# Optimization experiments

Measured on AMD Instinct MI355X. Metric: run time of the kernel, lower is better.

The kernel has to match this reference:

```python
import jax, jax.numpy as jnp
import numpy as np
from math import pi

BS, H, C = 4096, 1024, 512
H2, C2 = H // 2, C // 2


def _cm(x, y):
    # complex multiply with real/imag stored in last dim
    return jnp.stack([x[..., 0] * y[..., 0] - x[..., 1] * y[..., 1],
                      x[..., 0] * y[..., 1] + x[..., 1] * y[..., 0]], -1)


def _interleave(a, b):
    # (H2, C2),(H2, C2) -> (H, C2) rows [a0,b0,a1,b1,...]
    return jnp.stack([a, b], 1).reshape(-1, a.shape[1])


def _rotations(phi, theta):
    cp, sp = jnp.cos(phi), jnp.sin(phi)
    ct, st = jnp.cos(theta), jnp.sin(theta)
    z = jnp.zeros_like(ct)
    diag = jnp.stack([_interleave(cp * ct, ct), _interleave(sp * ct, z)], -1)      # (H, C2, 2)
    offd = jnp.stack([_interleave(-cp * st, st), _interleave(-sp * st, z)], -1)    # (H, C2, 2)
    return diag.transpose(1, 0, 2), offd.transpose(1, 0, 2)                        # (C2, H, 2)


def _swap_pairs(x):
    # swap elements within adjacent pairs along the hidden axis
    bs, h, _ = x.shape
    return x.reshape(bs, h // 2, 2, 2)[:, :, ::-1, :].reshape(bs, h, 2)


def setup_inputs() -> dict:
    key = jax.random.key(0)
    ks = jax.random.split(key, 5)
    x = jax.random.normal(ks[0], (BS, H, 2), dtype=jnp.float32)
    phi0 = 2 * pi * jax.random.normal(ks[1], (H2, C2), dtype=jnp.float32)
    theta0 = 2 * pi * jax.random.normal(ks[2], (H2, C2), dtype=jnp.float32)
    phi1 = 2 * pi * jax.random.normal(ks[3], (H2, C2), dtype=jnp.float32)
    theta1 = 2 * pi * jax.random.normal(ks[4], (H2, C2), dtype=jnp.float32)
    return {"x": x, "phi0": phi0, "theta0": theta0, "phi1": phi1, "theta1": theta1}


def reference(x, phi0, theta0, phi1, theta1):
    d0, o0 = _rotations(phi0, theta0)
    d1, o1 = _rotations(phi1, theta1)

    def step(xc, dd):
        dd0, oo0, dd1, oo1 = dd
        xc = _cm(xc, dd0) + _cm(_swap_pairs(xc), oo0)
        xc = jnp.roll(xc, -1, axis=1)   # cat(x[1:], x[:1])
        xc = _cm(xc, dd1) + _cm(_swap_pairs(xc), oo1)
        xc = jnp.roll(xc, 1, axis=1)    # cat(x[-1:], x[:-1])
        return xc, None

    x, _ = jax.lax.scan(step, x, (d0, o0, d1, o1))
    return x
```

## Files before the change

### kernel.cpp

```cpp
#include <hip/hip_runtime.h>


#define H_DIM 1024
#define C2 256
#define RPW 2


__global__ __launch_bounds__(256) void eunn_coef_kernel(
    const float* __restrict__ phi0, const float* __restrict__ theta0,
    const float* __restrict__ phi1, const float* __restrict__ theta1,
    float4* __restrict__ coef) {
    int t = blockIdx.x * 256 + threadIdx.x;
    int i = t & 511;
    int p = (t >> 9) & 1;
    int c = t >> 10;
    const float* phi   = p ? phi1   : phi0;
    const float* theta = p ? theta1 : theta0;
    float ph = phi[i * C2 + c];
    float th = theta[i * C2 + c];
    float sp, cp, st, ct;
    __sincosf(ph, &sp, &cp);
    __sincosf(th, &st, &ct);
    int j = i & 7;
    int l = i >> 3;
    coef[(((c * 2 + p) * 8) + j) * 64 + l] = make_float4(ct, st, cp, sp);
}

__device__ __forceinline__ void rot_pair(const float4 q,
                                         float& ur, float& ui,
                                         float& wr, float& wi) {
    float ar = fmaf(-q.y, wr, q.x * ur);
    float ai = fmaf(-q.y, wi, q.x * ui);
    float br = fmaf( q.x, wr, q.y * ur);
    float bi = fmaf( q.x, wi, q.y * ui);
    ur = fmaf(-q.w, ai, q.z * ar);
    ui = fmaf( q.w, ar, q.z * ai);
    wr = br;
    wi = bi;
}

__global__ __launch_bounds__(256, 2) void eunn_main_kernel(
    const float* __restrict__ x,
    const float4* __restrict__ coef,
    float* __restrict__ out) {
    const int lane = threadIdx.x & 63;
    const int wave = threadIdx.x >> 6;
    const int row0 = (blockIdx.x * 4 + wave) * RPW;

    float vr[RPW][16], vi[RPW][16];

#pragma unroll
    for (int r = 0; r < RPW; ++r) {
        const float4* src = (const float4*)(x + (size_t)(row0 + r) * (H_DIM * 2)) + lane * 8;
#pragma unroll
        for (int m = 0; m < 8; ++m) {
            float4 f = src[m];
            vr[r][2 * m]     = f.x; vi[r][2 * m]     = f.y;
            vr[r][2 * m + 1] = f.z; vi[r][2 * m + 1] = f.w;
        }
    }

    const float4* cl = coef + lane;

#pragma unroll 1
    for (int c = 0; c < C2; ++c) {
        const float4* ca = cl + (size_t)c * 1024;

        float4 qq = ca[15 * 64];
        float qpx = __shfl(qq.x, (lane + 63) & 63);
        float qpy = __shfl(qq.y, (lane + 63) & 63);

        {
            float4 q0 = ca[0 * 64];
            float4 q7 = ca[7 * 64];
#pragma unroll
            for (int r = 0; r < RPW; ++r) {
                rot_pair(q0, vr[r][0],  vi[r][0],  vr[r][1],  vi[r][1]);
                rot_pair(q7, vr[r][14], vi[r][14], vr[r][15], vi[r][15]);
            }
        }
        float nbr[RPW], nbi[RPW], pbr[RPW], pbi[RPW];
#pragma unroll
        for (int r = 0; r < RPW; ++r) {
            nbr[r] = __shfl(vr[r][0],  (lane + 1)  & 63);
            nbi[r] = __shfl(vi[r][0],  (lane + 1)  & 63);
            pbr[r] = __shfl(vr[r][15], (lane + 63) & 63);
            pbi[r] = __shfl(vi[r][15], (lane + 63) & 63);
        }

#pragma unroll
        for (int j = 1; j < 7; ++j) {
            float4 q = ca[j * 64];
#pragma unroll
            for (int r = 0; r < RPW; ++r) {
                rot_pair(q, vr[r][2 * j],     vi[r][2 * j],
                            vr[r][2 * j + 1], vi[r][2 * j + 1]);
            }
        }

#pragma unroll
        for (int j = 0; j < 7; ++j) {
            float4 q = ca[(8 + j) * 64];
#pragma unroll
            for (int r = 0; r < RPW; ++r) {
                rot_pair(q, vr[r][2 * j + 1], vi[r][2 * j + 1],
                            vr[r][2 * j + 2], vi[r][2 * j + 2]);
            }
        }

#pragma unroll
        for (int r = 0; r < RPW; ++r) {
            float ar = fmaf(-qq.y, nbr[r], qq.x * vr[r][15]);
            float ai = fmaf(-qq.y, nbi[r], qq.x * vi[r][15]);
            vr[r][15] = fmaf(-qq.w, ai, qq.z * ar);
            vi[r][15] = fmaf( qq.w, ar, qq.z * ai);
            float b0r = fmaf(qpx, vr[r][0], qpy * pbr[r]);
            float b0i = fmaf(qpx, vi[r][0], qpy * pbi[r]);
            vr[r][0] = b0r; vi[r][0] = b0i;
        }
    }

#pragma unroll
    for (int r = 0; r < RPW; ++r) {
        float4* dst = (float4*)(out + (size_t)(row0 + r) * (H_DIM * 2)) + lane * 8;
#pragma unroll
        for (int m = 0; m < 8; ++m) {
            dst[m] = make_float4(vr[r][2 * m],     vi[r][2 * m],
                                 vr[r][2 * m + 1], vi[r][2 * m + 1]);
        }
    }
}

extern "C" void kernel_launch(void* const* d_in, const int* in_sizes, int n_in,
                              void* d_out, int out_size, void* d_ws, size_t ws_size,
                              hipStream_t stream) {
    const float* x      = (const float*)d_in[0];
    const float* phi0   = (const float*)d_in[1];
    const float* theta0 = (const float*)d_in[2];
    const float* phi1   = (const float*)d_in[3];
    const float* theta1 = (const float*)d_in[4];
    float* out = (float*)d_out;
    float4* coef = (float4*)d_ws;

    hipLaunchKernelGGL(eunn_coef_kernel, dim3(1024), dim3(256), 0, stream,
                       phi0, theta0, phi1, theta1, coef);

    hipLaunchKernelGGL(eunn_main_kernel, dim3(512), dim3(256), 0, stream,
                       x, coef, out);
}
```

Before: 426.1 us.

## Stage per-step rotation coefficients in double-buffered LDS via async global-to-LDS loads

The main kernel now copies each step's 16KB coefficient slice into shared memory with global_load_lds, prefetching step c+1 into the other half of a double buffer while step c is computed. All four waves of a block read from LDS instead of each wave fetching the same coefficients from global memory. A block-wide barrier is added every step. The coefficient kernel's thread mapping is also changed so that reads of phi/theta are coalesced along c, while the output layout stays the same. This trades redundant global and L2 traffic and load latency for per-step synchronisation and 32KB of LDS per block.

After: 441.6 us. 3.6% more time.

```diff
diff --git a/kernel.cpp b/kernel.cpp
--- a/kernel.cpp
+++ b/kernel.cpp
@@ -11,9 +11,10 @@
     const float* __restrict__ phi1, const float* __restrict__ theta1,
     float4* __restrict__ coef) {
     int t = blockIdx.x * 256 + threadIdx.x;
-    int i = t & 511;
-    int p = (t >> 9) & 1;
-    int c = t >> 10;
+    int c = t & 255;
+    int ip = t >> 8;
+    int i = ip >> 1;
+    int p = ip & 1;
     const float* phi   = p ? phi1   : phi0;
     const float* theta = p ? theta1 : theta0;
     float ph = phi[i * C2 + c];
@@ -21,9 +22,9 @@
     float sp, cp, st, ct;
     __sincosf(ph, &sp, &cp);
     __sincosf(th, &st, &ct);
-    int j = i & 7;
+    int j = (i & 7) + 8 * p;
     int l = i >> 3;
-    coef[(((c * 2 + p) * 8) + j) * 64 + l] = make_float4(ct, st, cp, sp);
+    coef[((c * 16) + j) * 64 + l] = make_float4(ct, st, cp, sp);
 }
 
 __device__ __forceinline__ void rot_pair(const float4 q,
@@ -43,8 +44,11 @@
     const float* __restrict__ x,
     const float4* __restrict__ coef,
     float* __restrict__ out) {
-    const int lane = threadIdx.x & 63;
-    const int wave = threadIdx.x >> 6;
+    __shared__ float lds[8192];
+
+    const int t = threadIdx.x;
+    const int lane = t & 63;
+    const int wave = t >> 6;
     const int row0 = (blockIdx.x * 4 + wave) * RPW;
 
     float vr[RPW][16], vi[RPW][16];
@@ -60,19 +64,40 @@
         }
     }
 
-    const float4* cl = coef + lane;
+    {
+        const char* g = (const char*)coef + (size_t)t * 16;
+        float* l = lds + t * 4;
+#pragma unroll
+        for (int k = 0; k < 4; ++k) {
+            __builtin_amdgcn_global_load_lds(
+                (const __attribute__((address_space(1))) void*)(g + k * 4096),
+                (__attribute__((address_space(3))) void*)(l + k * 1024), 16, 0, 0);
+        }
+    }
+    __syncthreads();
 
 #pragma unroll 1
     for (int c = 0; c < C2; ++c) {
-        const float4* ca = cl + (size_t)c * 1024;
+        if (c + 1 < C2) {
+            const char* g = (const char*)coef + (size_t)(c + 1) * 16384 + (size_t)t * 16;
+            float* l = lds + ((c + 1) & 1) * 4096 + t * 4;
+#pragma unroll
+            for (int k = 0; k < 4; ++k) {
+                __builtin_amdgcn_global_load_lds(
+                    (const __attribute__((address_space(1))) void*)(g + k * 4096),
+                    (__attribute__((address_space(3))) void*)(l + k * 1024), 16, 0, 0);
+            }
+        }
 
-        float4 qq = ca[15 * 64];
+        const float4* lq = (const float4*)(lds + (c & 1) * 4096) + lane;
+
+        float4 qq = lq[15 * 64];
         float qpx = __shfl(qq.x, (lane + 63) & 63);
         float qpy = __shfl(qq.y, (lane + 63) & 63);
 
         {
-            float4 q0 = ca[0 * 64];
-            float4 q7 = ca[7 * 64];
+            float4 q0 = lq[0 * 64];
+            float4 q7 = lq[7 * 64];
 #pragma unroll
             for (int r = 0; r < RPW; ++r) {
                 rot_pair(q0, vr[r][0],  vi[r][0],  vr[r][1],  vi[r][1]);
@@ -90,7 +115,7 @@
 
 #pragma unroll
         for (int j = 1; j < 7; ++j) {
-            float4 q = ca[j * 64];
+            float4 q = lq[j * 64];
 #pragma unroll
             for (int r = 0; r < RPW; ++r) {
                 rot_pair(q, vr[r][2 * j],     vi[r][2 * j],
@@ -100,7 +125,7 @@
 
 #pragma unroll
         for (int j = 0; j < 7; ++j) {
-            float4 q = ca[(8 + j) * 64];
+            float4 q = lq[(8 + j) * 64];
 #pragma unroll
             for (int r = 0; r < RPW; ++r) {
                 rot_pair(q, vr[r][2 * j + 1], vi[r][2 * j + 1],
@@ -118,6 +143,8 @@
             float b0i = fmaf(qpx, vi[r][0], qpy * pbi[r]);
             vr[r][0] = b0r; vi[r][0] = b0i;
         }
+
+        __syncthreads();
     }
 
 #pragma unroll
```
